# Performance work log

Measured on AMD Instinct MI355X. Metric: run time of the kernel, lower is better.

## Reference

```python
import jax, jax.numpy as jnp
import numpy as np

D_MODEL = 1024
NUM_TILES = 8
BATCH = 4096
TEMPERATURE = 0.5

gelu = lambda x: jax.nn.gelu(x, approximate=False)  # torch nn.GELU default = exact erf


def setup_inputs() -> dict:
    key = jax.random.key(0)
    ks = jax.random.split(key, 12)
    d, t = D_MODEL, NUM_TILES
    s = lambda fan_in: 1.0 / np.sqrt(fan_in)
    return {
        "x": jax.random.normal(ks[0], (BATCH, d), jnp.float32),
        # router: Linear(d,d) -> GELU -> Linear(d,num_tiles); weights stored (in,out)
        "Wr1": jax.random.uniform(ks[1], (d, d), jnp.float32, -s(d), s(d)),
        "br1": jax.random.uniform(ks[2], (d,), jnp.float32, -s(d), s(d)),
        "Wr2": jax.random.uniform(ks[3], (d, t), jnp.float32, -s(d), s(d)),
        "br2": jax.random.uniform(ks[4], (t,), jnp.float32, -s(d), s(d)),
        # tile nets: Linear(d,2d) -> GELU -> Linear(2d,d), stacked over tiles
        "W1": jax.random.uniform(ks[5], (t, d, 2 * d), jnp.float32, -s(d), s(d)),
        "b1": jax.random.uniform(ks[6], (t, 2 * d), jnp.float32, -s(d), s(d)),
        "W2": jax.random.uniform(ks[7], (t, 2 * d, d), jnp.float32, -s(2 * d), s(2 * d)),
        "b2": jax.random.uniform(ks[8], (t, d), jnp.float32, -s(2 * d), s(2 * d)),
        # output projection Linear(d,d)
        "Wo": jax.random.uniform(ks[9], (d, d), jnp.float32, -s(d), s(d)),
        "bo": jax.random.uniform(ks[10], (d,), jnp.float32, -s(d), s(d)),
    }


def reference(x, Wr1, br1, Wr2, br2, W1, b1, W2, b2, Wo, bo):
    # router logits / temperature
    route_logits = (gelu(x @ Wr1 + br1) @ Wr2 + br2) / TEMPERATURE  # (B, T)
    tile_idx = jnp.argmax(route_logits, axis=-1)                    # (B,)

    # hard routing: compute all tile MLPs, then select the argmax tile per token
    # (dense equivalent of per-sample dispatch; same math as the torch loop)
    h = gelu(jnp.einsum("bd,tdf->btf", x, W1) + b1[None])           # (B, T, 2d)
    tile_out = jnp.einsum("btf,tfd->btd", h, W2) + b2[None]         # (B, T, d)
    selected = jnp.take_along_axis(tile_out, tile_idx[:, None, None], axis=1)[:, 0]  # (B, d)

    output = selected @ Wo + bo                                     # (B, d)
    return output, tile_idx, route_logits
```

## Files before the change

kernel.cpp:

```cpp
#include <hip/hip_runtime.h>
#include <hip/hip_bf16.h>
#include <math.h>
#include <stdint.h>

typedef __bf16 bf16_t;
typedef __bf16 bf16x8 __attribute__((ext_vector_type(8)));
typedef float  f32x4  __attribute__((ext_vector_type(4)));

#define BATCH   4096
#define DM      1024
#define DFF     2048
#define NTILES  8
#define MAXXB   40

__device__ __forceinline__ float gelu_exact(float x) {
    return 0.5f * x * (1.0f + erff(x * 0.70710678118654752440f));
}

__device__ __forceinline__ void async_ld16(const bf16_t* g, bf16_t* l) {
    __builtin_amdgcn_global_load_lds(
        (const __attribute__((address_space(1))) void*)g,
        (__attribute__((address_space(3))) void*)l, 16, 0, 0);
}

__device__ __forceinline__ f32x4 mfma16(bf16x8 a, bf16x8 b, f32x4 c) {
    return __builtin_amdgcn_mfma_f32_16x16x32_bf16(a, b, c, 0, 0, 0);
}

template<bool LO>
__device__ void tconv64_body(const float* __restrict__ src, bf16_t* __restrict__ outh,
                             bf16_t* __restrict__ outl, int K, int N, int kt, int nt,
                             float4* t , int tid) {
    const int k0 = kt * 64, n0 = nt * 64;
#pragma unroll
    for (int p = 0; p < 4; ++p) {
        int row = p * 16 + (tid >> 4);
        int c = tid & 15;
        float4 v = *(const float4*)(src + (size_t)(k0 + row) * N + n0 + c * 4);
        t[row * 16 + (c ^ ((row >> 2) & 15))] = v;
    }
    __syncthreads();
    const int n = tid >> 2, b = tid & 3;
    const float* tf = (const float*)t;
    float v[16];
#pragma unroll
    for (int i = 0; i < 16; ++i) {
        int k = 16 * b + i;
        int f4 = k * 16 + ((n >> 2) ^ ((k >> 2) & 15));
        v[i] = tf[f4 * 4 + (n & 3)];
    }
    bf16x8 h0, h1;
#pragma unroll
    for (int i = 0; i < 8; ++i) { h0[i] = (bf16_t)v[i]; h1[i] = (bf16_t)v[8 + i]; }
    size_t oi = (size_t)(n0 + n) * K + k0 + 16 * b;
    *(bf16x8*)(outh + oi) = h0;
    *(bf16x8*)(outh + oi + 8) = h1;
    if constexpr (LO) {
        bf16x8 l0, l1;
#pragma unroll
        for (int i = 0; i < 8; ++i) {
            l0[i] = (bf16_t)(v[i] - (float)h0[i]);
            l1[i] = (bf16_t)(v[8 + i] - (float)h1[i]);
        }
        *(bf16x8*)(outl + oi) = l0;
        *(bf16x8*)(outl + oi + 8) = l1;
    }
}

#define NCVT2 2048
#define PREP_A_GRID (NCVT2 + 256)

__global__ __launch_bounds__(256) void prep_a_kernel(
    const float* __restrict__ x, const float* __restrict__ Wr1,
    bf16_t* __restrict__ xh, bf16_t* __restrict__ xl,
    bf16_t* __restrict__ Wr1h, bf16_t* __restrict__ Wr1l) {
    __shared__ float4 t[64 * 16];
    int b = blockIdx.x;
    if (b < NCVT2) {
        size_t i = (size_t)b * 256 + threadIdx.x;
        const float4* x4 = (const float4*)x;
        float4 v0 = x4[2 * i], v1 = x4[2 * i + 1];
        float f[8] = {v0.x, v0.y, v0.z, v0.w, v1.x, v1.y, v1.z, v1.w};
        bf16x8 h, l;
#pragma unroll
        for (int j = 0; j < 8; ++j) { h[j] = (bf16_t)f[j]; l[j] = (bf16_t)(f[j] - (float)h[j]); }
        *(bf16x8*)(xh + i * 8) = h;
        *(bf16x8*)(xl + i * 8) = l;
        return;
    }
    b -= NCVT2;
    tconv64_body<true>(Wr1, Wr1h, Wr1l, DM, DM, b >> 4, b & 15, t, threadIdx.x);
}

template<bool SPLIT, bool GATHER, bool GELU, bool SCATTER, bool OUTF32, int BK>
__device__ __forceinline__ void gemm_body(
    const bf16_t* __restrict__ A, const bf16_t* __restrict__ Alo,
    const bf16_t* __restrict__ Bt, const bf16_t* __restrict__ Btlo,
    const float* __restrict__ bias,
    float* __restrict__ outF, bf16_t* __restrict__ outB,
    const int* __restrict__ perm, const int* __restrict__ counts,
    int M, int N, int K, int bx, int by,
    bf16_t* As, bf16_t* Bs, bf16_t* Asl, bf16_t* Bsl) {
    constexpr int NCH = BK / 32;
    constexpr int CH  = 128 * 32;
    constexpr int BUF = NCH * CH;

    int tile = 0, rb, cnt = M;
    const int* permT = nullptr;
    if constexpr (GATHER) {
        int xb = bx, t = 0, c = 0;
        while (t < NTILES) {
            c = counts[t];
            int nbk = (c + 127) >> 7;
            if (xb < nbk) break;
            xb -= nbk; ++t;
        }
        if (t == NTILES) return;
        tile = t;
        rb = xb * 128;
        cnt = c;
        permT = perm + tile * BATCH;
    } else {
        rb = bx * 128;
    }
    Bt   += (size_t)tile * K * N;
    if constexpr (SPLIT) Btlo += (size_t)tile * K * N;
    bias += (size_t)tile * N;

    const int lane = threadIdx.x & 63;
    const int wave = threadIdx.x >> 6;
    const int wm = wave & 1, wn = wave >> 1;
    const int nb = by * 128;

    const int srow = lane >> 2;
    const int scol = ((lane & 3) ^ (srow & 3)) * 8;
    const int row = wave * 16 + srow;
    int arow;
    if constexpr (GATHER) {
        int pos = rb + row;
        if (pos > cnt - 1) pos = cnt - 1;
        arow = permT[pos];
    } else {
        arow = rb + row;
    }
    const size_t aoff = (size_t)arow * K + scol;
    const size_t boff = (size_t)(nb + row) * K + scol;

    f32x4 acc[4][2];
#pragma unroll
    for (int i = 0; i < 4; ++i)
#pragma unroll
        for (int j = 0; j < 2; ++j) acc[i][j] = (f32x4){0.f, 0.f, 0.f, 0.f};

    const int lr = lane & 15, lq = lane >> 4;
    const int rdoff = (lr * 4 + (lq ^ (lr & 3))) * 8;

    auto stage = [&](int k0, int buf) {
#pragma unroll
        for (int c = 0; c < NCH; ++c) {
            async_ld16(A  + aoff + k0 + c * 32, &As[buf * BUF + c * CH + wave * 512]);
            async_ld16(Bt + boff + k0 + c * 32, &Bs[buf * BUF + c * CH + wave * 512]);
            if constexpr (SPLIT) {
                async_ld16(Alo  + aoff + k0 + c * 32, &Asl[buf * BUF + c * CH + wave * 512]);
                async_ld16(Btlo + boff + k0 + c * 32, &Bsl[buf * BUF + c * CH + wave * 512]);
            }
        }
    };

    auto compute = [&](int cur) {
#pragma unroll
        for (int kk = 0; kk < NCH; ++kk) {
            const int base = cur * BUF + kk * CH;
            bf16x8 af[4], bfr[2], afl[4], bfl[2];
#pragma unroll
            for (int i = 0; i < 4; ++i) {
                af[i] = *(const bf16x8*)&As[base + (wm * 4 + i) * 512 + rdoff];
                if constexpr (SPLIT)
                    afl[i] = *(const bf16x8*)&Asl[base + (wm * 4 + i) * 512 + rdoff];
            }
#pragma unroll
            for (int j = 0; j < 2; ++j) {
                bfr[j] = *(const bf16x8*)&Bs[base + (wn * 2 + j) * 512 + rdoff];
                if constexpr (SPLIT)
                    bfl[j] = *(const bf16x8*)&Bsl[base + (wn * 2 + j) * 512 + rdoff];
            }
#pragma unroll
            for (int i = 0; i < 4; ++i)
#pragma unroll
                for (int j = 0; j < 2; ++j) {
                    acc[i][j] = mfma16(af[i], bfr[j], acc[i][j]);
                    if constexpr (SPLIT) {
                        acc[i][j] = mfma16(af[i], bfl[j], acc[i][j]);
                        acc[i][j] = mfma16(afl[i], bfr[j], acc[i][j]);
                    }
                }
        }
    };

    stage(0, 0);
    int cur = 0;
    for (int k0 = 0; k0 < K; k0 += BK, cur ^= 1) {
        __syncthreads();
        if (k0 + BK < K) stage(k0 + BK, cur ^ 1);
        compute(cur);
    }

#pragma unroll
    for (int i = 0; i < 4; ++i) {
#pragma unroll
        for (int j = 0; j < 2; ++j) {
#pragma unroll
            for (int r = 0; r < 4; ++r) {
                int m = wm * 64 + i * 16 + lq * 4 + r;
                int n = wn * 32 + j * 16 + lr;
                int pos = rb + m;
                if constexpr (GATHER) { if (pos >= cnt) continue; }
                int grow;
                if constexpr (SCATTER) grow = permT[pos];
                else                   grow = pos;
                int gn = nb + n;
                float v = acc[i][j][r] + bias[gn];
                if constexpr (GELU) v = gelu_exact(v);
                if constexpr (OUTF32) outF[(size_t)grow * N + gn] = v;
                else                  outB[(size_t)grow * N + gn] = (bf16_t)v;
            }
        }
    }
}

#define NTCONV_TILES (4096 + 4096 + 256)
#define R1F_GRID (256 + NTCONV_TILES / 2)

__global__ __launch_bounds__(512) void r1_fused_kernel(
    const bf16_t* __restrict__ xh, const bf16_t* __restrict__ xl,
    const bf16_t* __restrict__ Wr1h, const bf16_t* __restrict__ Wr1l,
    const float* __restrict__ br1, float* __restrict__ Hr,
    const float* __restrict__ W1, const float* __restrict__ W2,
    const float* __restrict__ Wo,
    bf16_t* __restrict__ W1t, bf16_t* __restrict__ W2t, bf16_t* __restrict__ Wot) {
    __shared__ __align__(16) bf16_t smem[32768];
    const int bid = blockIdx.x;
    if (bid < 256) {
        gemm_body<true, false, true, false, true, 32>(
            xh, xl, Wr1h, Wr1l, br1, Hr, nullptr, nullptr, nullptr,
            BATCH, DM, DM, bid & 31, bid >> 5,
            smem, smem + 8192, smem + 16384, smem + 24576);
        return;
    }
    const int tix = bid - 256;
    const int half = threadIdx.x >> 8;
    const int tid = threadIdx.x & 255;
    float4* t = (float4*)smem + half * 1024;
    const int tile = tix * 2 + half;
    if (tile < 4096) {
        int mat = tile >> 9, r = tile & 511;
        size_t off = (size_t)mat * DM * DFF;
        tconv64_body<false>(W1 + off, W1t + off, nullptr, DM, DFF, r >> 5, r & 31, t, tid);
    } else if (tile < 8192) {
        int tt = tile - 4096;
        int mat = tt >> 9, r = tt & 511;
        size_t off = (size_t)mat * DM * DFF;
        tconv64_body<false>(W2 + off, W2t + off, nullptr, DFF, DM, r >> 4, r & 15, t, tid);
    } else {
        int r = tile - 8192;
        tconv64_body<false>(Wo, Wot, nullptr, DM, DM, r >> 4, r & 15, t, tid);
    }
}

template<bool SPLIT, bool GATHER, bool GELU, bool SCATTER, bool OUTF32>
__global__ __launch_bounds__(512) void gemm_kernel(
    const bf16_t* __restrict__ A, const bf16_t* __restrict__ Alo,
    const bf16_t* __restrict__ Bt, const bf16_t* __restrict__ Btlo,
    const float* __restrict__ bias,
    float* __restrict__ outF, bf16_t* __restrict__ outB,
    const int* __restrict__ perm, const int* __restrict__ counts,
    int M, int N, int K) {
    constexpr int E = 2 * 2 * 128 * 32;
    __shared__ __align__(16) bf16_t As[E];
    __shared__ __align__(16) bf16_t Bs[E];
    __shared__ __align__(16) bf16_t Asl[SPLIT ? E : 8];
    __shared__ __align__(16) bf16_t Bsl[SPLIT ? E : 8];
    gemm_body<SPLIT, GATHER, GELU, SCATTER, OUTF32, 64>(
        A, Alo, Bt, Btlo, bias, outF, outB, perm, counts,
        M, N, K, blockIdx.x, blockIdx.y, As, Bs, Asl, Bsl);
}

__global__ __launch_bounds__(256) void router2_kernel(
    const float* __restrict__ Hr, const float* __restrict__ Wr2, const float* __restrict__ br2,
    float* __restrict__ outLog, float* __restrict__ outIdx,
    int* __restrict__ counts, int* __restrict__ perm) {
    __shared__ float w2s[DM * 9];
    __shared__ int h[NTILES], base[NTILES];
    const int tid = threadIdx.x;
    if (tid < NTILES) h[tid] = 0;
    for (int e = tid; e < DM * 8; e += 256) {
        int k = e >> 3, j = e & 7;
        w2s[k * 9 + j] = Wr2[e];
    }
    __syncthreads();

    const int lane = tid & 63, wave = tid >> 6;
    const int sub = lane >> 4;
    const int lr16 = lane & 15;
    const int row = blockIdx.x * 16 + wave * 4 + sub;

    const float4* Hr4 = (const float4*)Hr;
    float acc[8];
#pragma unroll
    for (int j = 0; j < 8; ++j) acc[j] = 0.f;

#pragma unroll
    for (int i = 0; i < 16; ++i) {
        int f = lr16 + i * 16;
        float4 hv = Hr4[(size_t)row * 256 + f];
        float hx[4] = {hv.x, hv.y, hv.z, hv.w};
        int kbase = f * 4;
#pragma unroll
        for (int d = 0; d < 4; ++d) {
            float xv = hx[d];
            const float* w = &w2s[(kbase + d) * 9];
#pragma unroll
            for (int j = 0; j < 8; ++j) acc[j] += xv * w[j];
        }
    }
#pragma unroll
    for (int off = 8; off; off >>= 1)
#pragma unroll
        for (int j = 0; j < 8; ++j) acc[j] += __shfl_down(acc[j], off);

    int bi = 0, rank = 0;
    if (lr16 == 0) {
        float best = -1e30f;
        float lg[8];
#pragma unroll
        for (int j = 0; j < 8; ++j) {
            float v = (acc[j] + br2[j]) * 2.0f;
            lg[j] = v;
            if (v > best) { best = v; bi = j; }
        }
        float4 lo = {lg[0], lg[1], lg[2], lg[3]};
        float4 hi = {lg[4], lg[5], lg[6], lg[7]};
        *(float4*)(outLog + (size_t)row * 8)     = lo;
        *(float4*)(outLog + (size_t)row * 8 + 4) = hi;
        outIdx[row] = (float)bi;
        rank = atomicAdd(&h[bi], 1);
    }
    __syncthreads();
    if (tid < NTILES && h[tid] > 0) base[tid] = atomicAdd(&counts[tid], h[tid]);
    __syncthreads();
    if (lr16 == 0) perm[bi * BATCH + base[bi] + rank] = row;
}

extern "C" void kernel_launch(void* const* d_in, const int* in_sizes, int n_in,
                              void* d_out, int out_size, void* d_ws, size_t ws_size,
                              hipStream_t stream) {
    const float* x   = (const float*)d_in[0];
    const float* Wr1 = (const float*)d_in[1];
    const float* br1 = (const float*)d_in[2];
    const float* Wr2 = (const float*)d_in[3];
    const float* br2 = (const float*)d_in[4];
    const float* W1  = (const float*)d_in[5];
    const float* b1  = (const float*)d_in[6];
    const float* W2  = (const float*)d_in[7];
    const float* b2  = (const float*)d_in[8];
    const float* Wo  = (const float*)d_in[9];
    const float* bo  = (const float*)d_in[10];

    char* ws = (char*)d_ws;
    size_t o = 0;
    auto carve = [&](size_t bytes) { char* p = ws + o; o = (o + bytes + 255) & ~(size_t)255; return p; };
    bf16_t* Wr1h = (bf16_t*)carve((size_t)DM * DM * 2);
    bf16_t* Wr1l = (bf16_t*)carve((size_t)DM * DM * 2);
    bf16_t* Wot  = (bf16_t*)carve((size_t)DM * DM * 2);
    bf16_t* W1t  = (bf16_t*)carve((size_t)NTILES * DM * DFF * 2);
    bf16_t* W2t  = (bf16_t*)carve((size_t)NTILES * DM * DFF * 2);
    bf16_t* xh   = (bf16_t*)carve((size_t)BATCH * DM * 2);
    bf16_t* xl   = (bf16_t*)carve((size_t)BATCH * DM * 2);
    bf16_t* H1   = (bf16_t*)carve((size_t)BATCH * DFF * 2);
    bf16_t* sel  = (bf16_t*)carve((size_t)BATCH * DM * 2);
    float*  Hr   = (float*)carve((size_t)BATCH * DM * 4);
    int*    counts = (int*)carve(NTILES * sizeof(int));
    int*    perm   = (int*)carve((size_t)NTILES * BATCH * sizeof(int));

    float* outMain = (float*)d_out;
    float* outIdx  = outMain + (size_t)BATCH * DM;
    float* outLog  = outIdx + BATCH;

    hipMemsetAsync(counts, 0, NTILES * sizeof(int), stream);

    prep_a_kernel<<<PREP_A_GRID, 256, 0, stream>>>(x, Wr1, xh, xl, Wr1h, Wr1l);

    r1_fused_kernel<<<R1F_GRID, 512, 0, stream>>>(xh, xl, Wr1h, Wr1l, br1, Hr,
                                                  W1, W2, Wo, W1t, W2t, Wot);

    router2_kernel<<<BATCH / 16, 256, 0, stream>>>(Hr, Wr2, br2, outLog, outIdx, counts, perm);

    gemm_kernel<false, true, true, true, false><<<dim3(MAXXB, DFF / 128, 1), 512, 0, stream>>>(
        xh, nullptr, W1t, nullptr, b1, nullptr, H1, perm, counts, BATCH, DFF, DM);

    gemm_kernel<false, true, false, true, false><<<dim3(MAXXB, DM / 128, 1), 512, 0, stream>>>(
        H1, nullptr, W2t, nullptr, b2, nullptr, sel, perm, counts, BATCH, DM, DFF);

    gemm_kernel<false, false, false, false, true><<<dim3(BATCH / 128, DM / 128, 1), 512, 0, stream>>>(
        sel, nullptr, Wot, nullptr, bo, outMain, nullptr, nullptr, nullptr, BATCH, DM, DM);
}
```

Before: 340.1 us.

## Replace gemm kernel with intra-block K-split GEMM reducing partials through LDS

Adds a new GEMM kernel that takes a 128x128 tile with 8 waves. Each group of four waves computes 2x2 64x64 subtiles over one half of each 64-wide K chunk, and the two halves are summed through LDS at the end. Each wave issues 16 MFMAs per step with larger register fragments, meant to raise MFMA density and cut per-step overhead compared with the previous gemm_body path. The cost is an extra LDS reduction and barrier, plus half the waves sitting idle during the epilogue.

```diff
diff --git a/kernel.cpp b/kernel.cpp
--- a/kernel.cpp
+++ b/kernel.cpp
@@ -267,22 +267,137 @@
     }
 }
 
-template<bool SPLIT, bool GATHER, bool GELU, bool SCATTER, bool OUTF32>
-__global__ __launch_bounds__(512) void gemm_kernel(
-    const bf16_t* __restrict__ A, const bf16_t* __restrict__ Alo,
-    const bf16_t* __restrict__ Bt, const bf16_t* __restrict__ Btlo,
+template<bool GATHER, bool GELU, bool SCATTER, bool OUTF32>
+__global__ __launch_bounds__(512) void gemm_ks_kernel(
+    const bf16_t* __restrict__ A, const bf16_t* __restrict__ Bt,
     const float* __restrict__ bias,
     float* __restrict__ outF, bf16_t* __restrict__ outB,
     const int* __restrict__ perm, const int* __restrict__ counts,
     int M, int N, int K) {
-    constexpr int E = 2 * 2 * 128 * 32;
-    __shared__ __align__(16) bf16_t As[E];
-    __shared__ __align__(16) bf16_t Bs[E];
-    __shared__ __align__(16) bf16_t Asl[SPLIT ? E : 8];
-    __shared__ __align__(16) bf16_t Bsl[SPLIT ? E : 8];
-    gemm_body<SPLIT, GATHER, GELU, SCATTER, OUTF32, 64>(
-        A, Alo, Bt, Btlo, bias, outF, outB, perm, counts,
-        M, N, K, blockIdx.x, blockIdx.y, As, Bs, Asl, Bsl);
+    constexpr int CH  = 128 * 32;
+    constexpr int BUF = 2 * CH;
+    __shared__ __align__(16) bf16_t As[2 * BUF];
+    __shared__ __align__(16) bf16_t Bs[2 * BUF];
+
+    int tile = 0, rb, cnt = M;
+    const int* permT = nullptr;
+    if constexpr (GATHER) {
+        int xb = blockIdx.x, t = 0, c = 0;
+        while (t < NTILES) {
+            c = counts[t];
+            int nbk = (c + 127) >> 7;
+            if (xb < nbk) break;
+            xb -= nbk; ++t;
+        }
+        if (t == NTILES) return;
+        tile = t;
+        rb = xb * 128;
+        cnt = c;
+        permT = perm + tile * BATCH;
+    } else {
+        rb = blockIdx.x * 128;
+    }
+    Bt   += (size_t)tile * K * N;
+    bias += (size_t)tile * N;
+
+    const int lane = threadIdx.x & 63;
+    const int wave = threadIdx.x >> 6;
+    const int wm = wave & 1, wn = (wave >> 1) & 1;
+    const int h  = wave >> 2;
+    const int nb = blockIdx.y * 128;
+
+    const int srow = lane >> 2;
+    const int scol = ((lane & 3) ^ (srow & 3)) * 8;
+    const int row = wave * 16 + srow;
+    int arow;
+    if constexpr (GATHER) {
+        int pos = rb + row;
+        if (pos > cnt - 1) pos = cnt - 1;
+        arow = permT[pos];
+    } else {
+        arow = rb + row;
+    }
+    const size_t aoff = (size_t)arow * K + scol;
+    const size_t boff = (size_t)(nb + row) * K + scol;
+
+    f32x4 acc[4][4];
+#pragma unroll
+    for (int i = 0; i < 4; ++i)
+#pragma unroll
+        for (int j = 0; j < 4; ++j) acc[i][j] = (f32x4){0.f, 0.f, 0.f, 0.f};
+
+    const int lr = lane & 15, lq = lane >> 4;
+    const int rdoff = (lr * 4 + (lq ^ (lr & 3))) * 8;
+
+    auto stage = [&](int k0, int buf) {
+#pragma unroll
+        for (int c = 0; c < 2; ++c) {
+            async_ld16(A  + aoff + k0 + c * 32, &As[buf * BUF + c * CH + wave * 512]);
+            async_ld16(Bt + boff + k0 + c * 32, &Bs[buf * BUF + c * CH + wave * 512]);
+        }
+    };
+
+    stage(0, 0);
+    int cur = 0;
+    for (int k0 = 0; k0 < K; k0 += 64, cur ^= 1) {
+        __syncthreads();
+        if (k0 + 64 < K) stage(k0 + 64, cur ^ 1);
+        const int base = cur * BUF + h * CH;
+        bf16x8 af[4], bf[4];
+#pragma unroll
+        for (int i = 0; i < 4; ++i)
+            af[i] = *(const bf16x8*)&As[base + (wm * 4 + i) * 512 + rdoff];
+#pragma unroll
+        for (int j = 0; j < 4; ++j)
+            bf[j] = *(const bf16x8*)&Bs[base + (wn * 4 + j) * 512 + rdoff];
+#pragma unroll
+        for (int i = 0; i < 4; ++i)
+#pragma unroll
+            for (int j = 0; j < 4; ++j)
+                acc[i][j] = mfma16(af[i], bf[j], acc[i][j]);
+    }
+
+    __syncthreads();
+    const int region = wn * 2 + wm;
+    float* rbuf = ((region & 2) ? (float*)Bs : (float*)As) + (region & 1) * 4096;
+    if (h == 1) {
+#pragma unroll
+        for (int i = 0; i < 4; ++i)
+#pragma unroll
+            for (int j = 0; j < 4; ++j)
+                *(f32x4*)&rbuf[(i * 4 + j) * 256 + lane * 4] = acc[i][j];
+    }
+    __syncthreads();
+    if (h == 1) return;
+#pragma unroll
+    for (int i = 0; i < 4; ++i)
+#pragma unroll
+        for (int j = 0; j < 4; ++j) {
+            f32x4 p = *(const f32x4*)&rbuf[(i * 4 + j) * 256 + lane * 4];
+            acc[i][j] += p;
+        }
+
+#pragma unroll
+    for (int i = 0; i < 4; ++i) {
+#pragma unroll
+        for (int j = 0; j < 4; ++j) {
+#pragma unroll
+            for (int r = 0; r < 4; ++r) {
+                int m = wm * 64 + i * 16 + lq * 4 + r;
+                int n = wn * 64 + j * 16 + lr;
+                int pos = rb + m;
+                if constexpr (GATHER) { if (pos >= cnt) continue; }
+                int grow;
+                if constexpr (SCATTER) grow = permT[pos];
+                else                   grow = pos;
+                int gn = nb + n;
+                float v = acc[i][j][r] + bias[gn];
+                if constexpr (GELU) v = gelu_exact(v);
+                if constexpr (OUTF32) outF[(size_t)grow * N + gn] = v;
+                else                  outB[(size_t)grow * N + gn] = (bf16_t)v;
+            }
+        }
+    }
 }
 
 __global__ __launch_bounds__(256) void router2_kernel(
@@ -395,12 +510,12 @@
 
     router2_kernel<<<BATCH / 16, 256, 0, stream>>>(Hr, Wr2, br2, outLog, outIdx, counts, perm);
 
-    gemm_kernel<false, true, true, true, false><<<dim3(MAXXB, DFF / 128, 1), 512, 0, stream>>>(
-        xh, nullptr, W1t, nullptr, b1, nullptr, H1, perm, counts, BATCH, DFF, DM);
-
-    gemm_kernel<false, true, false, true, false><<<dim3(MAXXB, DM / 128, 1), 512, 0, stream>>>(
-        H1, nullptr, W2t, nullptr, b2, nullptr, sel, perm, counts, BATCH, DM, DFF);
-
-    gemm_kernel<false, false, false, false, true><<<dim3(BATCH / 128, DM / 128, 1), 512, 0, stream>>>(
-        sel, nullptr, Wot, nullptr, bo, outMain, nullptr, nullptr, nullptr, BATCH, DM, DM);
-}
+    gemm_ks_kernel<true, true, true, false><<<dim3(MAXXB, DFF / 128, 1), 512, 0, stream>>>(
+        xh, W1t, b1, nullptr, H1, perm, counts, BATCH, DFF, DM);
+
+    gemm_ks_kernel<true, false, true, false><<<dim3(MAXXB, DM / 128, 1), 512, 0, stream>>>(
+        H1, W2t, b2, nullptr, sel, perm, counts, BATCH, DM, DFF);
+
+    gemm_ks_kernel<false, false, false, true><<<dim3(BATCH / 128, DM / 128, 1), 512, 0, stream>>>(
+        sel, Wot, bo, outMain, nullptr, nullptr, nullptr, BATCH, DM, DM);
+}
```

Result: slower. 390.5 us (+14.8%).
